# Performance work log

Measured on AMD Instinct MI355X. Metric: run time of the kernel, lower is better.

Reference implementation:

```python
import jax, jax.numpy as jnp
import numpy as np


def setup_inputs() -> dict:
    key = jax.random.key(0)
    k1, k2, k3, k4 = jax.random.split(key, 4)
    B, S, H, D = 4, 2048, 1024, 1024
    X = jax.random.normal(k1, (B, S, H), dtype=jnp.float32)
    # nn.Linear weight stored as [out, in]; we store as [in, out] for x @ W
    scale = 1.0 / np.sqrt(H)
    Wq = jax.random.normal(k2, (H, D), dtype=jnp.float32) * scale
    Wk = jax.random.normal(k3, (H, D), dtype=jnp.float32) * scale
    Wv = jax.random.normal(k4, (H, D), dtype=jnp.float32) * scale
    return {"X": X, "Wq": Wq, "Wk": Wk, "Wv": Wv}


def reference(X, Wq, Wk, Wv):
    B, S, H = X.shape
    q = X @ Wq  # [B, S, D]
    k = X @ Wk
    v = X @ Wv
    D = k.shape[-1]
    scores = jnp.einsum('bqd,bkd->bqk', q, k) / jnp.sqrt(jnp.float32(D))
    causal = jnp.tril(jnp.ones((S, S), dtype=bool))  # block_size mask sliced to S
    scores = jnp.where(causal, scores, -jnp.inf)
    weights = jax.nn.softmax(scores, axis=-1)  # dropout p=0.0 -> identity
    return jnp.einsum('bqk,bkd->bqd', weights, v)
```

## Files before the change

### kernel.cpp

```cpp
#include <hip/hip_runtime.h>

#define AS1 __attribute__((address_space(1)))
#define AS3 __attribute__((address_space(3)))

typedef __attribute__((ext_vector_type(8))) short short8;
typedef __attribute__((ext_vector_type(4))) float floatx4;

__device__ __forceinline__ short f2bf(float f) {
  union { float f; unsigned u; } v; v.f = f;
  return (short)((v.u + 0x7fffu + ((v.u >> 16) & 1u)) >> 16);
}
__device__ __forceinline__ float bf2f(short s) {
  union { unsigned u; float f; } v; v.u = ((unsigned)(unsigned short)s) << 16;
  return v.f;
}

__device__ __forceinline__ void gload_lds16(const void* g, void* l) {
  __builtin_amdgcn_global_load_lds((const AS1 unsigned*)g, (AS3 unsigned*)l, 16, 0, 0);
}

__device__ __forceinline__ void stage128x64(const short* __restrict__ G, long rowBase, long ld,
                                            int kBase, short* lds, int lane, int wave) {
  const short* gb = G + rowBase * ld + (long)kBase + (long)(lane >> 3) * ld + (lane & 7) * 8;
#pragma unroll
  for (int j = 0; j < 4; ++j) {
    int c = wave * 4 + j;
    gload_lds16(gb + (long)c * 8 * ld, lds + c * 512);
  }
}

__device__ __forceinline__ void mfma_step(const short* lA, const short* lB, floatx4 acc[4][4],
                                          int lane, int wm, int wn) {
#pragma unroll
  for (int kk = 0; kk < 64; kk += 32) {
    short8 a[4], b[4];
    int kq = kk + (lane >> 4) * 8;
#pragma unroll
    for (int i = 0; i < 4; ++i) {
      a[i] = *(const short8*)(lA + (wm * 64 + i * 16 + (lane & 15)) * 64 + kq);
      b[i] = *(const short8*)(lB + (wn * 64 + i * 16 + (lane & 15)) * 64 + kq);
    }
#pragma unroll
    for (int i = 0; i < 4; ++i)
#pragma unroll
      for (int j = 0; j < 4; ++j)
        acc[i][j] = __builtin_amdgcn_mfma_f32_16x16x32_bf16(a[i], b[j], acc[i][j], 0, 0, 0);
  }
}

__device__ const unsigned char PAIR_LUT[136] = {
  0x40,0x41,0x42,0x43,0x50,0x51,0x52,0x53,0x60,0x61,0x62,0x63,0x70,0x71,0x72,0x73,
  0x80,0x81,0x82,0x83,0x90,0x91,0x92,0x93,0xA0,0xA1,0xA2,0xA3,0xB0,0xB1,0xB2,0xB3,
  0x84,0x85,0x86,0x87,0x94,0x95,0x96,0x97,0xA4,0xA5,0xA6,0xA7,0xB4,0xB5,0xB6,0xB7,
  0xC0,0xC1,0xC2,0xC3,0xD0,0xD1,0xD2,0xD3,0xE0,0xE1,0xE2,0xE3,0xF0,0xF1,0xF2,0xF3,
  0xC4,0xC5,0xC6,0xC7,0xD4,0xD5,0xD6,0xD7,0xE4,0xE5,0xE6,0xE7,0xF4,0xF5,0xF6,0xF7,
  0xC8,0xC9,0xCA,0xCB,0xD8,0xD9,0xDA,0xDB,0xE8,0xE9,0xEA,0xEB,0xF8,0xF9,0xFA,0xFB,
  0x00,0x10,0x11,0x20,0x21,0x22,0x30,0x31,0x32,0x33,
  0x44,0x54,0x55,0x64,0x65,0x66,0x74,0x75,0x76,0x77,
  0x88,0x98,0x99,0xA8,0xA9,0xAA,0xB8,0xB9,0xBA,0xBB,
  0xCC,0xDC,0xDD,0xEC,0xED,0xEE,0xFC,0xFD,0xFE,0xFF
};

__global__ void prep_inputs(const float* __restrict__ X, const float* __restrict__ Wq,
                            const float* __restrict__ Wk, const float* __restrict__ Wv,
                            short* __restrict__ Xb, short* __restrict__ Wt,
                            float* __restrict__ l) {
  __shared__ float t[32][33];
  if (blockIdx.x < 8192) {
    long i = ((long)blockIdx.x * 256 + threadIdx.x) * 4;
    float4 v = *(const float4*)(X + i);
    short4 o;
    o.x = f2bf(v.x); o.y = f2bf(v.y); o.z = f2bf(v.z); o.w = f2bf(v.w);
    *(short4*)(Xb + i) = o;
  } else if (blockIdx.x < 11264) {
    int idx = blockIdx.x - 8192;
    int z = idx >> 10, rem = idx & 1023;
    int bx = rem >> 5, by = rem & 31;
    const float* W = z == 0 ? Wq : (z == 1 ? Wk : Wv);
    short* O = Wt + (long)z * 1024 * 1024;
    int tx = threadIdx.x & 31, ty = threadIdx.x >> 5;
    int x = bx * 32 + tx;
    int y0 = by * 32;
    for (int j = ty; j < 32; j += 8)
      t[j][tx] = W[(long)(y0 + j) * 1024 + x];
    __syncthreads();
    int x2 = by * 32 + tx;
    int y2 = bx * 32;
    for (int j = ty; j < 32; j += 8)
      O[(long)(y2 + j) * 1024 + x2] = f2bf(t[tx][j]);
  } else {
    l[(blockIdx.x - 11264) * 256 + threadIdx.x] = 0.0f;
  }
}

__global__ __launch_bounds__(256, 4) void gemm_qkv(const short* __restrict__ Xb,
                                                   const short* __restrict__ Wt,
                                                   short* __restrict__ Q, short* __restrict__ K2,
                                                   short* __restrict__ Vt) {
  __shared__ short lA[128 * 64], lB[128 * 64];
  const int lane = threadIdx.x & 63, wave = threadIdx.x >> 6;
  const int wm = wave >> 1, wn = wave & 1;
  const int z = blockIdx.z;
  const short* Bm = Wt + (long)z * 1024 * 1024;
  const long mBase = (long)blockIdx.x * 128;
  const long nBase = (long)blockIdx.y * 128;

  floatx4 acc[4][4];
  const floatx4 zero = {0.f, 0.f, 0.f, 0.f};
#pragma unroll
  for (int i = 0; i < 4; ++i)
#pragma unroll
    for (int j = 0; j < 4; ++j) acc[i][j] = zero;

  for (int kt = 0; kt < 16; ++kt) {
    stage128x64(Xb, mBase, 1024, kt * 64, lA, lane, wave);
    stage128x64(Bm, nBase, 1024, kt * 64, lB, lane, wave);
    __syncthreads();
    mfma_step(lA, lB, acc, lane, wm, wn);
    __syncthreads();
  }

  if (z < 2) {
    short* out = (z == 0) ? Q : K2;
#pragma unroll
    for (int i = 0; i < 4; ++i)
#pragma unroll
      for (int j = 0; j < 4; ++j) {
        int col = (int)nBase + wn * 64 + j * 16 + (lane & 15);
#pragma unroll
        for (int r = 0; r < 4; ++r) {
          long m = mBase + wm * 64 + i * 16 + (lane >> 4) * 4 + r;
          out[m * 1024 + col] = f2bf(acc[i][j][r]);
        }
      }
  } else {
    const long bb = mBase >> 11;
    const int sBase = (int)(mBase & 2047);
#pragma unroll
    for (int i = 0; i < 4; ++i) {
      int s0 = sBase + wm * 64 + i * 16 + ((lane >> 4) << 2);
#pragma unroll
      for (int j = 0; j < 4; ++j) {
        int col = (int)nBase + wn * 64 + j * 16 + (lane & 15);
        short4 o;
        o.x = f2bf(acc[i][j][0]); o.y = f2bf(acc[i][j][1]);
        o.z = f2bf(acc[i][j][2]); o.w = f2bf(acc[i][j][3]);
        *(short4*)(Vt + ((bb * 1024 + col) * 2048 + s0)) = o;
      }
    }
  }
}

__global__ __launch_bounds__(256, 4) void scores_exp(const short* __restrict__ Q,
                                                     const short* __restrict__ Kk,
                                                     short* __restrict__ E, float* __restrict__ l) {
  __shared__ short lbuf[16384];
  short* lA = lbuf;
  short* lB = lbuf + 8192;
  const int lane = threadIdx.x & 63, wave = threadIdx.x >> 6;
  const int wm = wave >> 1, wn = wave & 1;
  const int b = blockIdx.y;

  const int r = blockIdx.x & 7, w = blockIdx.x >> 3;
  const int code = PAIR_LUT[r * 17 + w];
  const int qt = code >> 4, kt = code & 15;

  const long rowQ = (long)b * 2048 + (long)qt * 128;
  const long rowK = (long)b * 2048 + (long)kt * 128;

  floatx4 acc[4][4];
  const floatx4 zero = {0.f, 0.f, 0.f, 0.f};
#pragma unroll
  for (int i = 0; i < 4; ++i)
#pragma unroll
    for (int j = 0; j < 4; ++j) acc[i][j] = zero;

  for (int it = 0; it < 16; ++it) {
    stage128x64(Q, rowQ, 1024, it * 64, lA, lane, wave);
    stage128x64(Kk, rowK, 1024, it * 64, lB, lane, wave);
    __syncthreads();
    mfma_step(lA, lB, acc, lane, wm, wn);
    __syncthreads();
  }

  float* lrow = l + (long)b * 2048;
#pragma unroll
  for (int i = 0; i < 4; ++i) {
#pragma unroll
    for (int rr = 0; rr < 4; ++rr) {
      int ri = wm * 64 + i * 16 + (lane >> 4) * 4 + rr;
      int qrow = qt * 128 + ri;
      float psum = 0.f;
#pragma unroll
      for (int j = 0; j < 4; ++j) {
        int ci = wn * 64 + j * 16 + (lane & 15);
        int col = kt * 128 + ci;
        float sc = acc[i][j][rr] * 0.03125f;
        float e = (col <= qrow) ? __expf(sc) : 0.0f;
        short eb = f2bf(e);
        lbuf[ri * 128 + ((((ci >> 3) ^ (ri & 15)) << 3) | (ci & 7))] = eb;
        psum += bf2f(eb);
      }
      for (int m = 1; m < 16; m <<= 1) psum += __shfl_xor(psum, m, 64);
      if ((lane & 15) == 0) atomicAdd(&lrow[qrow], psum);
    }
  }
  __syncthreads();

  short* Eb = E + (long)b * 4194304;
  const long ebase = (long)(qt * 128) * 2048 + kt * 128;
#pragma unroll
  for (int pp = 0; pp < 8; ++pp) {
    int g = pp * 256 + threadIdx.x;
    int row = g >> 4, c = g & 15;
    short8 v = *(const short8*)(lbuf + row * 128 + ((c ^ (row & 15)) << 3));
    *(short8*)(Eb + ebase + (long)row * 2048 + c * 8) = v;
  }
}

__global__ __launch_bounds__(256, 4) void pv_gemm(const short* __restrict__ E,
                                                  const short* __restrict__ Vt,
                                                  const float* __restrict__ l,
                                                  float* __restrict__ part,
                                                  float* __restrict__ out) {
  __shared__ short lA[128 * 64], lB[128 * 64];
  const int lane = threadIdx.x & 63, wave = threadIdx.x >> 6;
  const int wm = wave >> 1, wn = wave & 1;
  const int xx = blockIdx.x;
  const int dt = xx / 24;
  const int within = xx % 24;
  const int r = within & 7, wsel = within >> 3;
  const int b = blockIdx.y;

  int qt, it0, it1, mode;
  if (wsel == 2) {
    qt = r; it0 = 0; it1 = (qt + 1) * 2; mode = 0;
  } else {
    qt = 15 - r;
    const int T = (qt + 1) * 2, c0 = T >> 1;
    if (wsel == 0) { it0 = 0;  it1 = c0; mode = 1; }
    else           { it0 = c0; it1 = T;  mode = 2; }
  }

  const short* Eb = E + (long)b * 2048 * 2048;
  const short* Vb = Vt + (long)b * 1024 * 2048;
  const float* lrow = l + (long)b * 2048;

  floatx4 acc[4][4];
  const floatx4 zero = {0.f, 0.f, 0.f, 0.f};
#pragma unroll
  for (int i = 0; i < 4; ++i)
#pragma unroll
    for (int j = 0; j < 4; ++j) acc[i][j] = zero;

  for (int it = it0; it < it1; ++it) {
    stage128x64(Eb, (long)qt * 128, 2048, it * 64, lA, lane, wave);
    stage128x64(Vb, (long)dt * 128, 2048, it * 64, lB, lane, wave);
    __syncthreads();
    mfma_step(lA, lB, acc, lane, wm, wn);
    __syncthreads();
  }

  if (mode == 2) {
    float* P = part + ((((long)b * 8 + (qt - 8)) * 8 + dt) << 14);
#pragma unroll
    for (int i = 0; i < 4; ++i)
#pragma unroll
      for (int rr = 0; rr < 4; ++rr) {
        int ri = wm * 64 + i * 16 + (lane >> 4) * 4 + rr;
#pragma unroll
        for (int j = 0; j < 4; ++j) {
          int ci = wn * 64 + j * 16 + (lane & 15);
          P[ri * 128 + ci] = acc[i][j][rr];
        }
      }
  } else {
#pragma unroll
    for (int i = 0; i < 4; ++i)
#pragma unroll
      for (int rr = 0; rr < 4; ++rr) {
        int qrow = qt * 128 + wm * 64 + i * 16 + (lane >> 4) * 4 + rr;
        float scale = (mode == 0) ? 1.0f / lrow[qrow] : 1.0f;
#pragma unroll
        for (int j = 0; j < 4; ++j) {
          int d = dt * 128 + wn * 64 + j * 16 + (lane & 15);
          out[((long)b * 2048 + qrow) * 1024 + d] = acc[i][j][rr] * scale;
        }
      }
  }
}

__global__ void pv_reduce(float* __restrict__ out, const float* __restrict__ part,
                          const float* __restrict__ l) {
  const int idx = blockIdx.x;
  const int b = idx >> 10;
  const int row = 1024 + (idx & 1023);
  const int t = threadIdx.x;
  const int dt = t >> 5, dl = (t << 2) & 127;
  const float inv = 1.0f / l[((long)b << 11) + row];
  const long pbase = ((((long)b * 8 + ((row >> 7) - 8)) * 8 + dt) << 14) + ((row & 127) << 7) + dl;
  const long obase = (((long)b * 2048 + row) << 10) + (t << 2);
  float4 o = *(const float4*)(out + obase);
  float4 p = *(const float4*)(part + pbase);
  o.x = (o.x + p.x) * inv; o.y = (o.y + p.y) * inv;
  o.z = (o.z + p.z) * inv; o.w = (o.w + p.w) * inv;
  *(float4*)(out + obase) = o;
}

extern "C" void kernel_launch(void* const* d_in, const int* in_sizes, int n_in,
                              void* d_out, int out_size, void* d_ws, size_t ws_size,
                              hipStream_t stream) {
  const float* X  = (const float*)d_in[0];
  const float* Wq = (const float*)d_in[1];
  const float* Wk = (const float*)d_in[2];
  const float* Wv = (const float*)d_in[3];

  char* ws = (char*)d_ws;
  short* Xb = (short*)(ws);
  short* Wt = (short*)(ws + 16777216L);
  short* Q  = (short*)(ws + 23068672L);
  short* K2 = (short*)(ws + 39845888L);
  short* Vt = (short*)(ws + 56623104L);
  short* E  = (short*)(ws + 73400320L);
  float* l  = (float*)(ws + 106954752L);
  float* part = (float*)(ws);

  prep_inputs<<<11296, 256, 0, stream>>>(X, Wq, Wk, Wv, Xb, Wt, l);
  gemm_qkv<<<dim3(64, 8, 3), 256, 0, stream>>>(Xb, Wt, Q, K2, Vt);
  scores_exp<<<dim3(136, 4), 256, 0, stream>>>(Q, K2, E, l);
  pv_gemm<<<dim3(192, 4), 256, 0, stream>>>(E, Vt, l, part, (float*)d_out);
  pv_reduce<<<4096, 256, 0, stream>>>((float*)d_out, part, l);
}
```

Before: 239.8 us.

## Rewrite QKV GEMM as 256x256 double-buffered pipelined kernel with 8 waves

Replaces the 128x128 QKV projection GEMM with a 256x256 tile per 512-thread block. It double-buffers LDS using direct global-to-LDS loads, interleaving the staging of the next k-slice with MFMA phases separated by barriers and priority bumps. It also adds an XOR-swizzled LDS layout and a block-index swizzle for L2 locality. The goal is to hide load latency and raise operand reuse. In exchange the kernel uses 128KB of LDS and more accumulator registers per thread, which limits occupancy.

```diff
diff --git a/kernel.cpp b/kernel.cpp
--- a/kernel.cpp
+++ b/kernel.cpp
@@ -93,59 +93,171 @@
   }
 }
 
-__global__ __launch_bounds__(256, 4) void gemm_qkv(const short* __restrict__ Xb,
+#define LOFF(b, m, h) ((((b) * 2 + (m)) * 2 + (h)) * 8192)
+#define MEMFENCE() asm volatile("" ::: "memory")
+#define SBAR() do { MEMFENCE(); __builtin_amdgcn_s_barrier(); MEMFENCE(); } while (0)
+
+__device__ __forceinline__ void stage_half(const short* __restrict__ g, short* l, int wv) {
+  gload_lds16(g, l + wv * 512);
+  gload_lds16(g + 65536, l + 4096 + wv * 512);
+}
+
+__device__ __forceinline__ short8 lds_rd(const short* l, int row, int kk, int lane) {
+  const int r = row + (lane & 15);
+  const int c = (kk + ((lane >> 4) << 3)) ^ ((lane & 7) << 3);
+  return *(const short8*)(l + r * 64 + c);
+}
+
+__global__ __launch_bounds__(512, 2) void gemm_qkv(const short* __restrict__ Xb,
                                                    const short* __restrict__ Wt,
                                                    short* __restrict__ Q, short* __restrict__ K2,
                                                    short* __restrict__ Vt) {
-  __shared__ short lA[128 * 64], lB[128 * 64];
-  const int lane = threadIdx.x & 63, wave = threadIdx.x >> 6;
-  const int wm = wave >> 1, wn = wave & 1;
-  const int z = blockIdx.z;
-  const short* Bm = Wt + (long)z * 1024 * 1024;
-  const long mBase = (long)blockIdx.x * 128;
-  const long nBase = (long)blockIdx.y * 128;
-
-  floatx4 acc[4][4];
+  __shared__ __align__(16) short lds[65536];
+  const int tid = threadIdx.x;
+  const int lane = tid & 63, wv = tid >> 6;
+  const int wm = wv >> 2, wn = wv & 3;
+
+  const int bid = blockIdx.x;
+  const int swz = (bid & 7) * 48 + (bid >> 3);
+  const int mt = swz & 31, ng = swz >> 5;
+  const int z = ng >> 2;
+  const long mBase = (long)mt * 256;
+  const long nBase = (long)(ng & 3) * 256;
+  const short* Bm = Wt + (long)z * 1048576;
+
+  const int r0 = tid >> 3;
+  const int cc = ((tid & 7) ^ (r0 & 7)) << 3;
+  const short* gA = Xb + (mBase + r0) * 1024 + cc;
+  const short* gB = Bm + (nBase + r0) * 1024 + cc;
+
+  floatx4 acc[8][4];
   const floatx4 zero = {0.f, 0.f, 0.f, 0.f};
 #pragma unroll
-  for (int i = 0; i < 4; ++i)
+  for (int i = 0; i < 8; ++i)
 #pragma unroll
     for (int j = 0; j < 4; ++j) acc[i][j] = zero;
 
-  for (int kt = 0; kt < 16; ++kt) {
-    stage128x64(Xb, mBase, 1024, kt * 64, lA, lane, wave);
-    stage128x64(Bm, nBase, 1024, kt * 64, lB, lane, wave);
-    __syncthreads();
-    mfma_step(lA, lB, acc, lane, wm, wn);
-    __syncthreads();
+  stage_half(gA, lds + LOFF(0, 0, 0), wv);
+  stage_half(gA + 131072, lds + LOFF(0, 0, 1), wv);
+  stage_half(gB, lds + LOFF(0, 1, 0), wv);
+  stage_half(gB + 131072, lds + LOFF(0, 1, 1), wv);
+  stage_half(gA + 64, lds + LOFF(1, 0, 0), wv);
+  stage_half(gA + 64 + 131072, lds + LOFF(1, 0, 1), wv);
+  asm volatile("s_waitcnt vmcnt(4)" ::: "memory");
+  SBAR();
+
+#pragma unroll 2
+  for (int t = 0; t < 16; ++t) {
+    const int buf = t & 1;
+    const short* Ab = lds + LOFF(buf, 0, wm);
+    const short* Bb = lds + LOFF(buf, 1, (wn >> 1));
+    const int brow = (wn & 1) * 64;
+    short8 a0[4][2], a1[4][2], bq[2][2];
+
+#pragma unroll
+    for (int f = 0; f < 4; ++f) {
+      a0[f][0] = lds_rd(Ab, f * 16, 0, lane);
+      a0[f][1] = lds_rd(Ab, f * 16, 32, lane);
+    }
+#pragma unroll
+    for (int n = 0; n < 2; ++n) {
+      bq[n][0] = lds_rd(Bb, brow + n * 16, 0, lane);
+      bq[n][1] = lds_rd(Bb, brow + n * 16, 32, lane);
+    }
+    if (t < 15) stage_half(gB + (t + 1) * 64, lds + LOFF(buf ^ 1, 1, 0), wv);
+    SBAR();
+    asm volatile("s_waitcnt lgkmcnt(0)" ::: "memory");
+    __builtin_amdgcn_s_setprio(1);
+#pragma unroll
+    for (int f = 0; f < 4; ++f)
+#pragma unroll
+      for (int n = 0; n < 2; ++n) {
+        acc[f][n] = __builtin_amdgcn_mfma_f32_16x16x32_bf16(a0[f][0], bq[n][0], acc[f][n], 0, 0, 0);
+        acc[f][n] = __builtin_amdgcn_mfma_f32_16x16x32_bf16(a0[f][1], bq[n][1], acc[f][n], 0, 0, 0);
+      }
+    __builtin_amdgcn_s_setprio(0);
+    SBAR();
+
+#pragma unroll
+    for (int f = 0; f < 4; ++f) {
+      a1[f][0] = lds_rd(Ab, 64 + f * 16, 0, lane);
+      a1[f][1] = lds_rd(Ab, 64 + f * 16, 32, lane);
+    }
+    if (t < 15) stage_half(gB + (t + 1) * 64 + 131072, lds + LOFF(buf ^ 1, 1, 1), wv);
+    SBAR();
+    asm volatile("s_waitcnt lgkmcnt(0)" ::: "memory");
+    __builtin_amdgcn_s_setprio(1);
+#pragma unroll
+    for (int f = 0; f < 4; ++f)
+#pragma unroll
+      for (int n = 0; n < 2; ++n) {
+        acc[4 + f][n] = __builtin_amdgcn_mfma_f32_16x16x32_bf16(a1[f][0], bq[n][0], acc[4 + f][n], 0, 0, 0);
+        acc[4 + f][n] = __builtin_amdgcn_mfma_f32_16x16x32_bf16(a1[f][1], bq[n][1], acc[4 + f][n], 0, 0, 0);
+      }
+    __builtin_amdgcn_s_setprio(0);
+    SBAR();
+
+#pragma unroll
+    for (int n = 0; n < 2; ++n) {
+      bq[n][0] = lds_rd(Bb, brow + (2 + n) * 16, 0, lane);
+      bq[n][1] = lds_rd(Bb, brow + (2 + n) * 16, 32, lane);
+    }
+    if (t < 14) stage_half(gA + (t + 2) * 64, lds + LOFF(buf, 0, 0), wv);
+    SBAR();
+    asm volatile("s_waitcnt lgkmcnt(0)" ::: "memory");
+    __builtin_amdgcn_s_setprio(1);
+#pragma unroll
+    for (int f = 0; f < 4; ++f)
+#pragma unroll
+      for (int n = 0; n < 2; ++n) {
+        acc[f][2 + n] = __builtin_amdgcn_mfma_f32_16x16x32_bf16(a0[f][0], bq[n][0], acc[f][2 + n], 0, 0, 0);
+        acc[f][2 + n] = __builtin_amdgcn_mfma_f32_16x16x32_bf16(a0[f][1], bq[n][1], acc[f][2 + n], 0, 0, 0);
+      }
+    __builtin_amdgcn_s_setprio(0);
+    SBAR();
+
+    if (t < 14) stage_half(gA + (t + 2) * 64 + 131072, lds + LOFF(buf, 0, 1), wv);
+    SBAR();
+    __builtin_amdgcn_s_setprio(1);
+#pragma unroll
+    for (int f = 0; f < 4; ++f)
+#pragma unroll
+      for (int n = 0; n < 2; ++n) {
+        acc[4 + f][2 + n] = __builtin_amdgcn_mfma_f32_16x16x32_bf16(a1[f][0], bq[n][0], acc[4 + f][2 + n], 0, 0, 0);
+        acc[4 + f][2 + n] = __builtin_amdgcn_mfma_f32_16x16x32_bf16(a1[f][1], bq[n][1], acc[4 + f][2 + n], 0, 0, 0);
+      }
+    __builtin_amdgcn_s_setprio(0);
+    if (t < 14) { asm volatile("s_waitcnt vmcnt(4)" ::: "memory"); }
+    else        { asm volatile("s_waitcnt vmcnt(0)" ::: "memory"); }
+    SBAR();
   }
 
   if (z < 2) {
-    short* out = (z == 0) ? Q : K2;
-#pragma unroll
-    for (int i = 0; i < 4; ++i)
-#pragma unroll
-      for (int j = 0; j < 4; ++j) {
-        int col = (int)nBase + wn * 64 + j * 16 + (lane & 15);
-#pragma unroll
-        for (int r = 0; r < 4; ++r) {
-          long m = mBase + wm * 64 + i * 16 + (lane >> 4) * 4 + r;
-          out[m * 1024 + col] = f2bf(acc[i][j][r]);
+    short* outp = (z == 0) ? Q : K2;
+#pragma unroll
+    for (int f = 0; f < 8; ++f)
+#pragma unroll
+      for (int n = 0; n < 4; ++n) {
+        const int col = (int)nBase + wn * 64 + n * 16 + (lane & 15);
+#pragma unroll
+        for (int rr = 0; rr < 4; ++rr) {
+          const long m = mBase + wm * 128 + f * 16 + ((lane >> 4) << 2) + rr;
+          outp[m * 1024 + col] = f2bf(acc[f][n][rr]);
         }
       }
   } else {
-    const long bb = mBase >> 11;
-    const int sBase = (int)(mBase & 2047);
-#pragma unroll
-    for (int i = 0; i < 4; ++i) {
-      int s0 = sBase + wm * 64 + i * 16 + ((lane >> 4) << 2);
-#pragma unroll
-      for (int j = 0; j < 4; ++j) {
-        int col = (int)nBase + wn * 64 + j * 16 + (lane & 15);
+    const long bz = mBase >> 11;
+    const int sB = (int)(mBase & 2047);
+#pragma unroll
+    for (int f = 0; f < 8; ++f) {
+      const int s0 = sB + wm * 128 + f * 16 + ((lane >> 4) << 2);
+#pragma unroll
+      for (int n = 0; n < 4; ++n) {
+        const int col = (int)nBase + wn * 64 + n * 16 + (lane & 15);
         short4 o;
-        o.x = f2bf(acc[i][j][0]); o.y = f2bf(acc[i][j][1]);
-        o.z = f2bf(acc[i][j][2]); o.w = f2bf(acc[i][j][3]);
-        *(short4*)(Vt + ((bb * 1024 + col) * 2048 + s0)) = o;
+        o.x = f2bf(acc[f][n][0]); o.y = f2bf(acc[f][n][1]);
+        o.z = f2bf(acc[f][n][2]); o.w = f2bf(acc[f][n][3]);
+        *(short4*)(Vt + ((bz * 1024 + col) * 2048 + s0)) = o;
       }
     }
   }
@@ -326,7 +438,7 @@
   float* part = (float*)(ws);
 
   prep_inputs<<<11296, 256, 0, stream>>>(X, Wq, Wk, Wv, Xb, Wt, l);
-  gemm_qkv<<<dim3(64, 8, 3), 256, 0, stream>>>(Xb, Wt, Q, K2, Vt);
+  gemm_qkv<<<384, 512, 0, stream>>>(Xb, Wt, Q, K2, Vt);
   scores_exp<<<dim3(136, 4), 256, 0, stream>>>(Q, K2, E, l);
   pv_gemm<<<dim3(192, 4), 256, 0, stream>>>(E, Vt, l, part, (float*)d_out);
   pv_reduce<<<4096, 256, 0, stream>>>((float*)d_out, part, l);
```

After: 241.6 us. Within noise of the previous version (+0.8%).
